# Kernel optimization log

Hardware: AMD Instinct MI355X
Metric: run time of the kernel (lower is better)

## Reference

```python
import jax, jax.numpy as jnp
import numpy as np

N_ROWS = 32768
CHANNELS = 4096

def setup_inputs() -> dict:
    key = jax.random.key(0)
    k1, k2 = jax.random.split(key)
    x = jax.random.normal(k1, (N_ROWS, CHANNELS), dtype=jnp.float32)
    # nn.Parameter(torch.ones(channels)); use uniform in (0.5, 1.5) around init for a nontrivial test
    diagonal = jax.random.uniform(k2, (CHANNELS,), dtype=jnp.float32, minval=0.5, maxval=1.5)
    return {"x": x, "diagonal": diagonal}

def reference(x, diagonal):
    # torch.matmul(x, torch.diag_embed(diagonal)) == x * diagonal (broadcast over last axis)
    return x * diagonal
```

## Files before the change

kernel.cpp:

```cpp
#include <hip/hip_runtime.h>


#define CH4 1024

typedef float f32x4 __attribute__((ext_vector_type(4)));

template <bool HOIST>
__global__ __launch_bounds__(256)
void DiagonalLinear_80960133529733_kernel(const f32x4* __restrict__ x,
                                          const f32x4* __restrict__ diag,
                                          f32x4* __restrict__ out,
                                          unsigned int n4) {
    const unsigned int stride = gridDim.x * blockDim.x;
    unsigned int i = blockIdx.x * blockDim.x + threadIdx.x;

    f32x4 dv;
    if (HOIST) dv = diag[i & (CH4 - 1)];

    for (; i < n4; i += stride) {
        f32x4 xv = __builtin_nontemporal_load(&x[i]);
        f32x4 dvv = HOIST ? dv : diag[i & (CH4 - 1)];
        __builtin_nontemporal_store(xv * dvv, &out[i]);
    }
}

extern "C" void kernel_launch(void* const* d_in, const int* in_sizes, int n_in,
                              void* d_out, int out_size, void* d_ws, size_t ws_size,
                              hipStream_t stream) {
    const float* x    = (const float*)d_in[0];
    const float* diag = (const float*)d_in[1];
    float* out        = (float*)d_out;

    const long long n  = (long long)in_sizes[0];
    const unsigned int n4 = (unsigned int)(n / 4);

    const int block = 256;
    long long want = ((long long)n4 + block - 1) / block;
    int grid = (int)(want < 2048 ? want : 2048);

    const unsigned int stride = (unsigned int)grid * block;
    if ((stride & (CH4 - 1)) == 0) {
        DiagonalLinear_80960133529733_kernel<true><<<grid, block, 0, stream>>>(
            (const f32x4*)x, (const f32x4*)diag, (f32x4*)out, n4);
    } else {
        DiagonalLinear_80960133529733_kernel<false><<<grid, block, 0, stream>>>(
            (const f32x4*)x, (const f32x4*)diag, (f32x4*)out, n4);
    }
}
```

Baseline: 203.0 us.

## Use contiguous per-block chunks with four hoisted diagonal vectors

Adds a chunked kernel where each block streams a contiguous slice of the matrix instead of grid-striding across it. Each thread keeps the four diagonal vectors it needs in registers and processes four loads and stores per iteration. The goal is more sequential DRAM access per block and more memory operations in flight. The old grid-stride kernel stays as a fallback for sizes that do not divide evenly.

Measured after the change: 197.6 us. 1.03x faster.

```diff
diff --git a/kernel.cpp b/kernel.cpp
--- a/kernel.cpp
+++ b/kernel.cpp
@@ -5,18 +5,43 @@
 
 typedef float f32x4 __attribute__((ext_vector_type(4)));
 
+__global__ __launch_bounds__(256)
+void DiagonalLinear_chunked(const f32x4* __restrict__ x,
+                            const f32x4* __restrict__ diag,
+                            f32x4* __restrict__ out,
+                            unsigned int chunk) {
+    const unsigned int tid  = threadIdx.x;
+    const unsigned int base = blockIdx.x * chunk + tid;
+    const unsigned int iters = chunk >> 8;
+
+    const f32x4 d0 = diag[tid];
+    const f32x4 d1 = diag[tid + 256];
+    const f32x4 d2 = diag[tid + 512];
+    const f32x4 d3 = diag[tid + 768];
+
+    unsigned int idx = base;
+    for (unsigned int k = 0; k < iters; k += 4, idx += 1024) {
+        f32x4 a = __builtin_nontemporal_load(&x[idx]);
+        __builtin_nontemporal_store(a * d0, &out[idx]);
+        f32x4 b = __builtin_nontemporal_load(&x[idx + 256]);
+        __builtin_nontemporal_store(b * d1, &out[idx + 256]);
+        f32x4 c = __builtin_nontemporal_load(&x[idx + 512]);
+        __builtin_nontemporal_store(c * d2, &out[idx + 512]);
+        f32x4 d = __builtin_nontemporal_load(&x[idx + 768]);
+        __builtin_nontemporal_store(d * d3, &out[idx + 768]);
+    }
+}
+
 template <bool HOIST>
 __global__ __launch_bounds__(256)
-void DiagonalLinear_80960133529733_kernel(const f32x4* __restrict__ x,
-                                          const f32x4* __restrict__ diag,
-                                          f32x4* __restrict__ out,
-                                          unsigned int n4) {
+void DiagonalLinear_gs(const f32x4* __restrict__ x,
+                       const f32x4* __restrict__ diag,
+                       f32x4* __restrict__ out,
+                       unsigned int n4) {
     const unsigned int stride = gridDim.x * blockDim.x;
     unsigned int i = blockIdx.x * blockDim.x + threadIdx.x;
-
     f32x4 dv;
     if (HOIST) dv = diag[i & (CH4 - 1)];
-
     for (; i < n4; i += stride) {
         f32x4 xv = __builtin_nontemporal_load(&x[i]);
         f32x4 dvv = HOIST ? dv : diag[i & (CH4 - 1)];
@@ -35,15 +60,23 @@
     const unsigned int n4 = (unsigned int)(n / 4);
 
     const int block = 256;
-    long long want = ((long long)n4 + block - 1) / block;
-    int grid = (int)(want < 2048 ? want : 2048);
+    const int grid  = 2048;
+    const unsigned int chunk = n4 / grid;
 
-    const unsigned int stride = (unsigned int)grid * block;
-    if ((stride & (CH4 - 1)) == 0) {
-        DiagonalLinear_80960133529733_kernel<true><<<grid, block, 0, stream>>>(
-            (const f32x4*)x, (const f32x4*)diag, (f32x4*)out, n4);
+    if ((long long)grid * chunk == (long long)n4 &&
+        (chunk & (CH4 - 1)) == 0 && ((chunk >> 8) & 3) == 0) {
+        DiagonalLinear_chunked<<<grid, block, 0, stream>>>(
+            (const f32x4*)x, (const f32x4*)diag, (f32x4*)out, chunk);
     } else {
-        DiagonalLinear_80960133529733_kernel<false><<<grid, block, 0, stream>>>(
-            (const f32x4*)x, (const f32x4*)diag, (f32x4*)out, n4);
+        long long want = ((long long)n4 + block - 1) / block;
+        int g = (int)(want < 2048 ? want : 2048);
+        const unsigned int stride = (unsigned int)g * block;
+        if ((stride & (CH4 - 1)) == 0) {
+            DiagonalLinear_gs<true><<<g, block, 0, stream>>>(
+                (const f32x4*)x, (const f32x4*)diag, (f32x4*)out, n4);
+        } else {
+            DiagonalLinear_gs<false><<<g, block, 0, stream>>>(
+                (const f32x4*)x, (const f32x4*)diag, (f32x4*)out, n4);
+        }
     }
 }
```
